# Performance work log

Measured on AMD Instinct MI355X. Metric: run time of the kernel, lower is better.

Reference implementation:

```python
import jax, jax.numpy as jnp
import numpy as np

H_K, H_V, DK, DV = 8, 16, 128, 128
HIDDEN = 2048
KDIM, VDIM = H_K * DK, H_V * DV          # 1024, 2048
CONV_DIM = 2 * KDIM + VDIM               # 4096
KS = 4                                   # conv kernel size
EPS = 1e-6


def setup_inputs() -> dict:
    key = jax.random.key(0)
    ks = jax.random.split(key, 8)
    B, S = 1, 1024
    return {
        "hidden_states": jax.random.normal(ks[0], (B, S, HIDDEN), jnp.float32),
        "W_qkvz": jax.random.uniform(ks[1], (HIDDEN, 2 * KDIM + 2 * VDIM), jnp.float32, -0.25, 0.25) * 0.1,
        "W_ba": jax.random.uniform(ks[2], (HIDDEN, 2 * H_V), jnp.float32, -0.25, 0.25),
        "conv_w": jax.random.normal(ks[3], (CONV_DIM, KS), jnp.float32) * 0.1,
        "dt_bias": jnp.ones((H_V,), jnp.float32),
        "A_log": jnp.log(jax.random.uniform(ks[4], (H_V,), jnp.float32, 1e-4, 16.0)),
        "norm_weight": jnp.ones((DV,), jnp.float32),
        "W_out": jax.random.uniform(ks[5], (VDIM, HIDDEN), jnp.float32, -0.06, 0.06),
    }


def _split_qkvz_ba(qkvz, ba):
    # mimic fix_query_key_value_ordering: per-k-head interleaved layout
    B, S, _ = qkvz.shape
    vpk = H_V // H_K
    qkvz = qkvz.reshape(B, S, H_K, 2 * DK + 2 * vpk * DV)
    q = qkvz[..., :DK]
    k = qkvz[..., DK:2 * DK]
    v = qkvz[..., 2 * DK:2 * DK + vpk * DV].reshape(B, S, H_V, DV)
    z = qkvz[..., 2 * DK + vpk * DV:].reshape(B, S, H_V, DV)
    ba = ba.reshape(B, S, H_K, 2 * vpk)
    b = ba[..., :vpk].reshape(B, S, H_V)
    a = ba[..., vpk:].reshape(B, S, H_V)
    return q, k, v, z, b, a


def _causal_conv_silu(x, w):
    # x: [B, S, C] ; w: [C, K] depthwise causal conv, then SiLU
    xt = jnp.swapaxes(x, 1, 2)                      # [B, C, S]
    xt = jnp.pad(xt, ((0, 0), (0, 0), (KS - 1, 0)))
    y = jax.lax.conv_general_dilated(
        xt, w[:, None, :], (1,), 'VALID',
        dimension_numbers=('NCH', 'OIH', 'NCH'),
        feature_group_count=w.shape[0])
    return jax.nn.silu(jnp.swapaxes(y, 1, 2))       # [B, S, C]


def _l2norm(x):
    return x * jax.lax.rsqrt(jnp.sum(x * x, axis=-1, keepdims=True) + 1e-6)


def _gated_delta_rule(q, k, v, g, beta):
    # q, k: [B,S,H,DK]; v: [B,S,H,DV]; g, beta: [B,S,H]
    B, S, H, _ = q.shape
    scale = DK ** -0.5
    q = _l2norm(q) * scale
    k = _l2norm(k)
    qs = jnp.moveaxis(q, 1, 0)   # [S,B,H,DK]
    ks = jnp.moveaxis(k, 1, 0)
    vs = jnp.moveaxis(v, 1, 0)
    gs = jnp.moveaxis(g, 1, 0)   # [S,B,H]
    bs = jnp.moveaxis(beta, 1, 0)
    S0 = jnp.zeros((B, H, DK, DV), q.dtype)

    def step(St, xs):
        qt, kt, vt, gt, bt = xs
        St = St * jnp.exp(gt)[..., None, None]
        pred = jnp.einsum('bhk,bhkv->bhv', kt, St)
        delta = (vt - pred) * bt[..., None]
        St = St + jnp.einsum('bhk,bhv->bhkv', kt, delta)
        o = jnp.einsum('bhk,bhkv->bhv', qt, St)
        return St, o

    _, o = jax.lax.scan(step, S0, (qs, ks, vs, gs, bs))
    return jnp.moveaxis(o, 0, 1)  # [B,S,H,DV]


def _gated_rmsnorm(x, z, w):
    # FLA FusedRMSNormGated (silu): rmsnorm(x)*w, gated by silu(z)
    var = jnp.mean(x * x, axis=-1, keepdims=True)
    return (x * jax.lax.rsqrt(var + EPS)) * w * jax.nn.silu(z)


def _forward(hidden_states, W_qkvz, W_ba, conv_w, dt_bias, A_log, norm_weight, W_out):
    B, S, _ = hidden_states.shape
    qkvz = hidden_states @ W_qkvz
    ba = hidden_states @ W_ba
    q, k, v, z, b, a = _split_qkvz_ba(qkvz, ba)
    mixed = jnp.concatenate([q.reshape(B, S, KDIM), k.reshape(B, S, KDIM),
                             v.reshape(B, S, VDIM)], axis=-1)
    mixed = _causal_conv_silu(mixed, conv_w)
    q = mixed[..., :KDIM].reshape(B, S, H_K, DK)
    k = mixed[..., KDIM:2 * KDIM].reshape(B, S, H_K, DK)
    v = mixed[..., 2 * KDIM:].reshape(B, S, H_V, DV)
    beta = jax.nn.sigmoid(b)
    g = -jnp.exp(A_log) * jax.nn.softplus(a + dt_bias)   # [B,S,H_V]
    rep = H_V // H_K
    q = jnp.repeat(q, rep, axis=2)
    k = jnp.repeat(k, rep, axis=2)
    o = _gated_delta_rule(q, k, v, g, beta)              # [B,S,H_V,DV]
    o = _gated_rmsnorm(o, z, norm_weight)
    return o.reshape(B, S, VDIM) @ W_out


def reference(hidden_states, W_qkvz, W_ba, conv_w, dt_bias, A_log, norm_weight, W_out):
    return _forward(hidden_states, W_qkvz, W_ba, conv_w, dt_bias, A_log, norm_weight, W_out)
```

## Files before the change

### kernel.cpp

```cpp
#include <hip/hip_runtime.h>
#include <hip/hip_bf16.h>
#include <math.h>


#define SEQ 1024
#define HID 2048
#define NQKVZ 6144

typedef __attribute__((ext_vector_type(8))) short short8;
typedef __attribute__((ext_vector_type(4))) float f32x4;

__device__ __forceinline__ unsigned short f2bf(float f) {
  __hip_bfloat16 h = __float2bfloat16(f);
  return *reinterpret_cast<unsigned short*>(&h);
}
__device__ __forceinline__ float bf2f(unsigned short u) {
  unsigned int x = ((unsigned int)u) << 16;
  return __int_as_float(x);
}

typedef __attribute__((address_space(3))) void lds_void;
typedef const __attribute__((address_space(1))) void g_void;
__device__ __forceinline__ void gload16(const void* g, void* l) {
  __builtin_amdgcn_global_load_lds((g_void*)g, (lds_void*)l, 16, 0, 0);
}

__global__ __launch_bounds__(256) void cast_bf16(const float* __restrict__ in,
                                                 unsigned short* __restrict__ out,
                                                 int n) {
  const int i = (blockIdx.x * 256 + threadIdx.x) * 4;
  if (i < n) {
    const float4 v = *(const float4*)&in[i];
    ushort4 o;
    o.x = f2bf(v.x); o.y = f2bf(v.y); o.z = f2bf(v.z); o.w = f2bf(v.w);
    *(ushort4*)&out[i] = o;
  }
}

__global__ __launch_bounds__(256) void transpose_cast2(const float* __restrict__ W1,
                                                       unsigned short* __restrict__ W1t,
                                                       const float* __restrict__ W2,
                                                       unsigned short* __restrict__ W2t) {
  __shared__ float tile[32][33];
  int bx = blockIdx.x;
  const float* W;
  unsigned short* Wt;
  int N;
  if (bx < 192) { W = W1; Wt = W1t; N = NQKVZ; }
  else          { W = W2; Wt = W2t; N = HID; bx -= 192; }
  const int n0 = bx * 32, k0 = blockIdx.y * 32;
  const int tx = threadIdx.x & 31, ty = threadIdx.x >> 5;
#pragma unroll
  for (int r = 0; r < 32; r += 8)
    tile[ty + r][tx] = W[(size_t)(k0 + ty + r) * N + n0 + tx];
  __syncthreads();
#pragma unroll
  for (int r = 0; r < 32; r += 8)
    Wt[(size_t)(n0 + ty + r) * HID + k0 + tx] = f2bf(tile[tx][ty + r]);
}

__global__ __launch_bounds__(256) void transpose_f32(const float* __restrict__ W,
                                                     float* __restrict__ Wt,
                                                     int K, int N) {
  __shared__ float tile[32][33];
  const int n0 = blockIdx.x * 32, k0 = blockIdx.y * 32;
  const int tx = threadIdx.x & 31, ty = threadIdx.x >> 5;
#pragma unroll
  for (int r = 0; r < 32; r += 8)
    tile[ty + r][tx] = W[(size_t)(k0 + ty + r) * N + n0 + tx];
  __syncthreads();
#pragma unroll
  for (int r = 0; r < 32; r += 8)
    Wt[(size_t)(n0 + ty + r) * K + k0 + tx] = tile[tx][ty + r];
}

#define SWZ(row) ((KF == 1) ? (((row) >> 1) & 3) : ((row) & 7))

template <int MF, int NF, int KF>
__global__ __launch_bounds__(256) void gemm_bf16(const unsigned short* __restrict__ A,
                                                 const unsigned short* __restrict__ Bt,
                                                 float* __restrict__ C,
                                                 int M, int N, int K) {
  constexpr int BM = 32 * MF, BN = 32 * NF, BK = 32 * KF;
  constexpr int RB  = BK * 2;
  constexpr int APW = (BM * KF / 16) / 4;
  constexpr int BPW = (BN * KF / 16) / 4;
  constexpr int RPG = 16 / KF;
  __shared__ unsigned short As[2][BM * BK];
  __shared__ unsigned short Bs[2][BN * BK];

  const int tid  = threadIdx.x;
  const int lane = tid & 63;
  const int w    = tid >> 6;
  const int wm   = w >> 1, wn = w & 1;
  const int row0 = blockIdx.y * BM, col0 = blockIdx.x * BN;

  const int lrow  = (KF == 1) ? (lane >> 2) : (lane >> 3);
  const int lslot = lane & (4 * KF - 1);
  const int arow  = lane & 15;

  f32x4 acc[MF][NF];
#pragma unroll
  for (int m = 0; m < MF; ++m)
#pragma unroll
    for (int n = 0; n < NF; ++n) acc[m][n] = (f32x4){0.f, 0.f, 0.f, 0.f};

  auto stage = [&](int bi, int kt) {
    const int ko = kt * BK;
#pragma unroll
    for (int u = 0; u < APW; ++u) {
      const int gu = w * APW + u;
      const int row = gu * RPG + lrow;
      const int sg = lslot ^ SWZ(row);
      gload16(A + (size_t)(row0 + row) * K + ko + sg * 8,
              (char*)As[bi] + gu * 1024 + lane * 16);
    }
#pragma unroll
    for (int u = 0; u < BPW; ++u) {
      const int gu = w * BPW + u;
      const int row = gu * RPG + lrow;
      const int sg = lslot ^ SWZ(row);
      gload16(Bt + (size_t)(col0 + row) * K + ko + sg * 8,
              (char*)Bs[bi] + gu * 1024 + lane * 16);
    }
  };

  stage(0, 0);
  __syncthreads();

  int cur = 0;
  const int nk = K / BK;
  for (int kt = 0; kt < nk; ++kt) {
    if (kt + 1 < nk) stage(cur ^ 1, kt + 1);

    const char* asb = (const char*)As[cur];
    const char* bsb = (const char*)Bs[cur];
    short8 af[MF][KF], bf[NF][KF];
#pragma unroll
    for (int m = 0; m < MF; ++m)
#pragma unroll
      for (int kk = 0; kk < KF; ++kk) {
        const int row = wm * (16 * MF) + m * 16 + arow;
        const int slot = kk * 4 + (lane >> 4);
        af[m][kk] = *(const short8*)(asb + row * RB + ((slot ^ SWZ(row)) * 16));
      }
#pragma unroll
    for (int n = 0; n < NF; ++n)
#pragma unroll
      for (int kk = 0; kk < KF; ++kk) {
        const int row = wn * (16 * NF) + n * 16 + arow;
        const int slot = kk * 4 + (lane >> 4);
        bf[n][kk] = *(const short8*)(bsb + row * RB + ((slot ^ SWZ(row)) * 16));
      }
#pragma unroll
    for (int m = 0; m < MF; ++m)
#pragma unroll
      for (int n = 0; n < NF; ++n)
#pragma unroll
        for (int kk = 0; kk < KF; ++kk)
          acc[m][n] = __builtin_amdgcn_mfma_f32_16x16x32_bf16(af[m][kk], bf[n][kk],
                                                              acc[m][n], 0, 0, 0);

    __syncthreads();
    cur ^= 1;
  }

#pragma unroll
  for (int m = 0; m < MF; ++m)
#pragma unroll
    for (int n = 0; n < NF; ++n) {
      const int r0 = row0 + wm * (16 * MF) + m * 16 + (lane >> 4) * 4;
      const int c  = col0 + wn * (16 * NF) + n * 16 + (lane & 15);
#pragma unroll
      for (int r = 0; r < 4; ++r)
        C[(size_t)(r0 + r) * N + c] = acc[m][n][r];
    }
}

__global__ __launch_bounds__(256) void ba_kernel(const float* __restrict__ X,
                                                 const float* __restrict__ Wbt,
                                                 const float* __restrict__ A_log,
                                                 const float* __restrict__ dt_bias,
                                                 float* __restrict__ gbuf,
                                                 float* __restrict__ bet) {
  const int col = threadIdx.x & 31;
  const int kg  = threadIdx.x >> 5;
  const int s0  = blockIdx.x * 4;
  const float* wp = Wbt + (size_t)col * HID + kg * 256;
  const float* xp = X + (size_t)s0 * HID + kg * 256;

  float a0 = 0.f, a1 = 0.f, a2 = 0.f, a3 = 0.f;
  for (int kk = 0; kk < 256; kk += 4) {
    const float4 w4 = *(const float4*)&wp[kk];
    const float4 x0 = *(const float4*)&xp[kk];
    const float4 x1 = *(const float4*)&xp[kk + HID];
    const float4 x2 = *(const float4*)&xp[kk + 2 * HID];
    const float4 x3 = *(const float4*)&xp[kk + 3 * HID];
    a0 += x0.x * w4.x + x0.y * w4.y + x0.z * w4.z + x0.w * w4.w;
    a1 += x1.x * w4.x + x1.y * w4.y + x1.z * w4.z + x1.w * w4.w;
    a2 += x2.x * w4.x + x2.y * w4.y + x2.z * w4.z + x2.w * w4.w;
    a3 += x3.x * w4.x + x3.y * w4.y + x3.z * w4.z + x3.w * w4.w;
  }
  __shared__ float red[4][32][9];
  red[0][col][kg] = a0;
  red[1][col][kg] = a1;
  red[2][col][kg] = a2;
  red[3][col][kg] = a3;
  __syncthreads();
  if (threadIdx.x < 128) {
    const int r = threadIdx.x >> 5;
    const int c = threadIdx.x & 31;
    float acc = 0.f;
#pragma unroll
    for (int g = 0; g < 8; ++g) acc += red[r][c][g];
    const int s = s0 + r;
    const int hk = c >> 2, j = c & 3;
    if (j < 2) {
      bet[s * 16 + hk * 2 + j] = 1.f / (1.f + expf(-acc));
    } else {
      const int vh = hk * 2 + (j - 2);
      const float x = acc + dt_bias[vh];
      const float sp = (x > 20.f) ? x : log1pf(expf(x));
      gbuf[s * 16 + vh] = -expf(A_log[vh]) * sp;
    }
  }
}

#define NT 512
__global__ __launch_bounds__(NT) void chunk_prep(
    const float* __restrict__ qkvz, const float* __restrict__ conv_w,
    const float* __restrict__ gbuf, const float* __restrict__ bet,
    unsigned short* __restrict__ Tg, unsigned short* __restrict__ Gg,
    unsigned short* __restrict__ Wtg, unsigned short* __restrict__ Qtg,
    unsigned short* __restrict__ Khg, float* __restrict__ bvg,
    float* __restrict__ esg) {
  const int h  = blockIdx.x >> 4;
  const int c  = blockIdx.x & 15;
  const int hk = h >> 1;
  const int tid = threadIdx.x;
  const int lane = tid & 63;
  const int w    = tid >> 6;
  const int lr   = lane & 15;
  const int lk   = lane >> 4;

  __shared__ float raw[67][128];
  __shared__ unsigned short Kb[64 * 128];
  __shared__ unsigned short Qb[64 * 128];
  __shared__ unsigned short Bm[64][64];
  __shared__ float cg[64];
  __shared__ float btl[64];

  const int s0 = c * 64;
  const int qcol0 = hk * 768;
  const int kcol0 = hk * 768 + 128;
  const int vcol0 = hk * 768 + 256 + (h & 1) * 128;

  if (tid < 64) {
    float g = gbuf[(s0 + tid) * 16 + h];
#pragma unroll
    for (int d = 1; d < 64; d <<= 1) {
      const float o = __shfl_up(g, d);
      if (tid >= d) g += o;
    }
    cg[tid] = g;
    btl[tid] = bet[(s0 + tid) * 16 + h];
  }

  float4 rq[5], rk[5], rv[5];

#define ISSUE(col0_, rg)                                                      \
  _Pragma("unroll")                                                           \
  for (int ii = 0; ii < 5; ++ii) {                                            \
    const int idx = tid + NT * ii;                                            \
    if (idx < 67 * 32) {                                                      \
      const int r = idx >> 5, cq = (idx & 31) * 4;                            \
      const int sr = s0 - 3 + r;                                              \
      if (sr >= 0)                                                            \
        rg[ii] = *(const float4*)&qkvz[(size_t)sr * NQKVZ + (col0_) + cq];    \
      else { rg[ii].x = 0.f; rg[ii].y = 0.f; rg[ii].z = 0.f; rg[ii].w = 0.f; }\
    }                                                                         \
  }

#define WRITE(rg)                                                             \
  _Pragma("unroll")                                                           \
  for (int ii = 0; ii < 5; ++ii) {                                            \
    const int idx = tid + NT * ii;                                            \
    if (idx < 67 * 32) {                                                      \
      const int r = idx >> 5, cq = (idx & 31) * 4;                            \
      *(float4*)&raw[r][cq] = rg[ii];                                         \
    }                                                                         \
  }

#define CONV_TO(dst, wbase, isq)                                              \
  for (int n = 0; n < 4; ++n) {                                               \
    const int idx = tid + NT * n;                                             \
    const int row = idx >> 5;                                                 \
    const int col = (idx & 31) * 4;                                           \
    float wgt[4][4];                                                          \
    _Pragma("unroll")                                                         \
    for (int x = 0; x < 4; ++x) {                                             \
      const float4 a = *(const float4*)&conv_w[((wbase) + hk * 128 + col + x) * 4]; \
      wgt[x][0] = a.x; wgt[x][1] = a.y; wgt[x][2] = a.z; wgt[x][3] = a.w;     \
    }                                                                         \
    float4 ac = {0.f, 0.f, 0.f, 0.f};                                         \
    _Pragma("unroll")                                                         \
    for (int j = 0; j < 4; ++j) {                                             \
      const float4 xr = *(const float4*)&raw[row + j][col];                   \
      ac.x = fmaf(wgt[0][j], xr.x, ac.x); ac.y = fmaf(wgt[1][j], xr.y, ac.y); \
      ac.z = fmaf(wgt[2][j], xr.z, ac.z); ac.w = fmaf(wgt[3][j], xr.w, ac.w); \
    }                                                                         \
    float4 y;                                                                 \
    y.x = ac.x / (1.f + __expf(-ac.x)); y.y = ac.y / (1.f + __expf(-ac.y));   \
    y.z = ac.z / (1.f + __expf(-ac.z)); y.w = ac.w / (1.f + __expf(-ac.w));   \
    float ss = y.x * y.x + y.y * y.y + y.z * y.z + y.w * y.w;                 \
    _Pragma("unroll")                                                         \
    for (int m = 1; m <= 16; m <<= 1) ss += __shfl_xor(ss, m);                \
    float sc = rsqrtf(ss + 1e-6f);                                            \
    if (isq) sc *= 0.08838834764831845f;                                      \
    const int boff = row * 256 + ((col * 2) ^ ((row & 7) << 4));              \
    ushort4 o = {f2bf(y.x * sc), f2bf(y.y * sc), f2bf(y.z * sc), f2bf(y.w * sc)}; \
    *(ushort4*)((char*)(dst) + boff) = o;                                     \
  }

  ISSUE(qcol0, rq);
  WRITE(rq);
  __syncthreads();
  ISSUE(kcol0, rk);
  CONV_TO(Qb, 0, true);
  __syncthreads();
  WRITE(rk);
  __syncthreads();
  ISSUE(vcol0, rv);
  CONV_TO(Kb, 1024, false);
  __syncthreads();
  WRITE(rv);

  const bool isK = (w < 4);
  const int w4 = w & 3;
  f32x4 dacc[4];
#pragma unroll
  for (int ct = 0; ct < 4; ++ct) dacc[ct] = (f32x4){0.f, 0.f, 0.f, 0.f};
  {
    const int rowA = 16 * w4 + lr;
    const int swA  = (rowA & 7) << 4;
    const char* Ab = isK ? (const char*)Kb : (const char*)Qb;
#pragma unroll
    for (int ks = 0; ks < 4; ++ks) {
      const int kb = ks * 64 + lk * 16;
      const short8 a = *(const short8*)(Ab + rowA * 256 + (kb ^ swA));
#pragma unroll
      for (int ct = 0; ct < 4; ++ct) {
        const int rowB = ct * 16 + lr;
        const short8 bK = *(const short8*)((char*)Kb + rowB * 256 + (kb ^ ((rowB & 7) << 4)));
        dacc[ct] = __builtin_amdgcn_mfma_f32_16x16x32_bf16(a, bK, dacc[ct], 0, 0, 0);
      }
    }
  }
#pragma unroll
  for (int ct = 0; ct < 4; ++ct) {
#pragma unroll
    for (int r = 0; r < 4; ++r) {
      const int i = 16 * w4 + lk * 4 + r;
      const int j = ct * 16 + lr;
      const float e = __expf(cg[i] - cg[j]);
      if (isK) Bm[i][j] = f2bf((j < i) ? btl[i] * e * dacc[ct][r] : 0.f);
      else     Gg[(size_t)blockIdx.x * 4096 + i * 64 + j] =
                   f2bf((j <= i) ? e * dacc[ct][r] : 0.f);
    }
  }
  __syncthreads();

  const float cglast = cg[63];
  if (w == 0) {
    const int l = lane;
    float Tc[64];
#pragma unroll
    for (int i = 0; i < 64; ++i) {
      float v = (i == l) ? 1.f : 0.f;
#pragma unroll
      for (int j = 0; j < i; ++j) v -= bf2f(Bm[i][j]) * Tc[j];
      Tc[i] = v;
    }
#pragma unroll
    for (int i = 0; i < 64; ++i)
      Tg[(size_t)blockIdx.x * 4096 + i * 64 + l] = f2bf(Tc[i]);
    if (lane == 0) esg[blockIdx.x] = __expf(cglast);
  } else {
    const int t2 = tid - 64;
    for (int idx = t2; idx < 2048; idx += 448) {
      const int i = idx >> 5;
      const int dk = (idx & 31) * 4;
      const int boff = i * 256 + ((dk * 2) ^ ((i & 7) << 4));
      const ushort4 kq = *(const ushort4*)((char*)Kb + boff);
      const ushort4 qq = *(const ushort4*)((char*)Qb + boff);
      const float ei = __expf(cg[i]);
      const float wi = btl[i] * ei;
      ushort4 wo = {f2bf(wi * bf2f(kq.x)), f2bf(wi * bf2f(kq.y)),
                    f2bf(wi * bf2f(kq.z)), f2bf(wi * bf2f(kq.w))};
      ushort4 qo = {f2bf(ei * bf2f(qq.x)), f2bf(ei * bf2f(qq.y)),
                    f2bf(ei * bf2f(qq.z)), f2bf(ei * bf2f(qq.w))};
      *(ushort4*)&Wtg[(size_t)blockIdx.x * 8192 + i * 128 + dk] = wo;
      *(ushort4*)&Qtg[(size_t)blockIdx.x * 8192 + i * 128 + dk] = qo;

      float wv[4][4];
#pragma unroll
      for (int x = 0; x < 4; ++x) {
        const float4 a = *(const float4*)&conv_w[(2048 + h * 128 + dk + x) * 4];
        wv[x][0] = a.x; wv[x][1] = a.y; wv[x][2] = a.z; wv[x][3] = a.w;
      }
      float4 va = {0.f, 0.f, 0.f, 0.f};
#pragma unroll
      for (int j = 0; j < 4; ++j) {
        const float4 xv = *(const float4*)&raw[i + j][dk];
        va.x = fmaf(wv[0][j], xv.x, va.x); va.y = fmaf(wv[1][j], xv.y, va.y);
        va.z = fmaf(wv[2][j], xv.z, va.z); va.w = fmaf(wv[3][j], xv.w, va.w);
      }
      float4 bv4;
      bv4.x = btl[i] * va.x / (1.f + __expf(-va.x));
      bv4.y = btl[i] * va.y / (1.f + __expf(-va.y));
      bv4.z = btl[i] * va.z / (1.f + __expf(-va.z));
      bv4.w = btl[i] * va.w / (1.f + __expf(-va.w));
      *(float4*)&bvg[(size_t)blockIdx.x * 8192 + i * 128 + dk] = bv4;
    }
    for (int lin = t2; lin < 8192; lin += 448) {
      const int dk = lin >> 6, i = lin & 63;
      const unsigned short kraw =
          *(const unsigned short*)((char*)Kb + i * 256 + ((dk * 2) ^ ((i & 7) << 4)));
      Khg[(size_t)blockIdx.x * 8192 + lin] = f2bf(__expf(cglast - cg[i]) * bf2f(kraw));
    }
  }
#undef ISSUE
#undef WRITE
#undef CONV_TO
}
#undef NT

struct SFrags {
  short8 wf[4];
  short8 tf[2];
  short8 qf[4];
  short8 gf[2];
  short8 kh[2][2];
  float  bv[4];
  float  es;
};

__device__ __forceinline__ void sload(SFrags& F,
    const unsigned short* __restrict__ Tg, const unsigned short* __restrict__ Gg,
    const unsigned short* __restrict__ Wtg, const unsigned short* __restrict__ Qtg,
    const unsigned short* __restrict__ Khg, const float* __restrict__ bvg,
    const float* __restrict__ esg,
    size_t base, int w, int lr, int lk, int dv0) {
  const unsigned short* T_  = Tg  + base * 4096;
  const unsigned short* G_  = Gg  + base * 4096;
  const unsigned short* W_  = Wtg + base * 8192;
  const unsigned short* Q_  = Qtg + base * 8192;
  const unsigned short* Kh_ = Khg + base * 8192;
  const float* bv_ = bvg + base * 8192;
#pragma unroll
  for (int ks = 0; ks < 4; ++ks) {
    F.wf[ks] = *(const short8*)(W_ + (16 * w + lr) * 128 + ks * 32 + lk * 8);
    F.qf[ks] = *(const short8*)(Q_ + (16 * w + lr) * 128 + ks * 32 + lk * 8);
  }
#pragma unroll
  for (int ks = 0; ks < 2; ++ks) {
    F.tf[ks]    = *(const short8*)(T_ + (16 * w + lr) * 64 + ks * 32 + lk * 8);
    F.gf[ks]    = *(const short8*)(G_ + (16 * w + lr) * 64 + ks * 32 + lk * 8);
    F.kh[0][ks] = *(const short8*)(Kh_ + (32 * w + lr) * 64 + ks * 32 + lk * 8);
    F.kh[1][ks] = *(const short8*)(Kh_ + (32 * w + 16 + lr) * 64 + ks * 32 + lk * 8);
  }
#pragma unroll
  for (int r = 0; r < 4; ++r)
    F.bv[r] = bv_[(16 * w + lk * 4 + r) * 128 + dv0 + lr];
  F.es = esg[base];
}

__global__ __launch_bounds__(256) void scan_rec(
    const unsigned short* __restrict__ Tg, const unsigned short* __restrict__ Gg,
    const unsigned short* __restrict__ Wtg, const unsigned short* __restrict__ Qtg,
    const unsigned short* __restrict__ Khg, const float* __restrict__ bvg,
    const float* __restrict__ esg, float* __restrict__ obuf) {
  const int h   = blockIdx.x & 15;
  const int dvb = blockIdx.x >> 4;
  const int dv0 = dvb * 16;
  const int tid = threadIdx.x;
  const int lane = tid & 63;
  const int w   = tid >> 6;
  const int lr  = lane & 15;
  const int lk  = lane >> 4;

  __shared__ unsigned short Sb[16][136];
  __shared__ unsigned short Ub[16][72];
  __shared__ unsigned short Db[16][72];

  for (int n = tid; n < 16 * 136 / 2; n += 256) ((unsigned int*)Sb)[n] = 0u;

  f32x4 sacc0 = {0.f, 0.f, 0.f, 0.f};
  f32x4 sacc1 = {0.f, 0.f, 0.f, 0.f};

  SFrags fA, fB;
  sload(fA, Tg, Gg, Wtg, Qtg, Khg, bvg, esg, (size_t)h * 16, w, lr, lk, dv0);
  __syncthreads();

#define SCAN_CHUNK(F, c)                                                      \
  {                                                                           \
    short8 sb[4];                                                             \
    _Pragma("unroll")                                                         \
    for (int ks = 0; ks < 4; ++ks)                                            \
      sb[ks] = *(const short8*)(&Sb[lr][ks * 32 + lk * 8]);                   \
    f32x4 au = {0.f, 0.f, 0.f, 0.f};                                          \
    _Pragma("unroll")                                                         \
    for (int ks = 0; ks < 4; ++ks)                                            \
      au = __builtin_amdgcn_mfma_f32_16x16x32_bf16(F.wf[ks], sb[ks], au, 0, 0, 0); \
    {                                                                         \
      ushort4 pk;                                                             \
      _Pragma("unroll")                                                       \
      for (int r = 0; r < 4; ++r)                                             \
        ((unsigned short*)&pk)[r] = f2bf(F.bv[r] - au[r]);                    \
      *(ushort4*)&Ub[lr][16 * w + lk * 4] = pk;                               \
    }                                                                         \
    __syncthreads();                                                          \
    f32x4 ad = {0.f, 0.f, 0.f, 0.f};                                          \
    _Pragma("unroll")                                                         \
    for (int ks = 0; ks < 2; ++ks) {                                          \
      const short8 ub = *(const short8*)(&Ub[lr][ks * 32 + lk * 8]);          \
      ad = __builtin_amdgcn_mfma_f32_16x16x32_bf16(F.tf[ks], ub, ad, 0, 0, 0); \
    }                                                                         \
    {                                                                         \
      ushort4 pk;                                                             \
      _Pragma("unroll")                                                       \
      for (int r = 0; r < 4; ++r) ((unsigned short*)&pk)[r] = f2bf(ad[r]);    \
      *(ushort4*)&Db[lr][16 * w + lk * 4] = pk;                               \
    }                                                                         \
    __syncthreads();                                                          \
    short8 dbf[2];                                                            \
    _Pragma("unroll")                                                         \
    for (int ks = 0; ks < 2; ++ks)                                            \
      dbf[ks] = *(const short8*)(&Db[lr][ks * 32 + lk * 8]);                  \
    f32x4 ao = {0.f, 0.f, 0.f, 0.f};                                          \
    _Pragma("unroll")                                                         \
    for (int ks = 0; ks < 4; ++ks)                                            \
      ao = __builtin_amdgcn_mfma_f32_16x16x32_bf16(F.qf[ks], sb[ks], ao, 0, 0, 0); \
    _Pragma("unroll")                                                         \
    for (int ks = 0; ks < 2; ++ks)                                            \
      ao = __builtin_amdgcn_mfma_f32_16x16x32_bf16(F.gf[ks], dbf[ks], ao, 0, 0, 0); \
    _Pragma("unroll")                                                         \
    for (int r = 0; r < 4; ++r) {                                             \
      const int i = 16 * w + lk * 4 + r;                                      \
      obuf[((size_t)((c) * 64 + i) * 16 + h) * 128 + dv0 + lr] = ao[r];       \
    }                                                                         \
    sacc0 *= F.es;                                                            \
    sacc1 *= F.es;                                                            \
    _Pragma("unroll")                                                         \
    for (int ks = 0; ks < 2; ++ks) {                                          \
      sacc0 = __builtin_amdgcn_mfma_f32_16x16x32_bf16(F.kh[0][ks], dbf[ks], sacc0, 0, 0, 0); \
      sacc1 = __builtin_amdgcn_mfma_f32_16x16x32_bf16(F.kh[1][ks], dbf[ks], sacc1, 0, 0, 0); \
    }                                                                         \
    {                                                                         \
      ushort4 p0, p1;                                                         \
      _Pragma("unroll")                                                       \
      for (int r = 0; r < 4; ++r) {                                           \
        ((unsigned short*)&p0)[r] = f2bf(sacc0[r]);                           \
        ((unsigned short*)&p1)[r] = f2bf(sacc1[r]);                           \
      }                                                                       \
      *(ushort4*)&Sb[lr][32 * w + lk * 4] = p0;                               \
      *(ushort4*)&Sb[lr][32 * w + 16 + lk * 4] = p1;                          \
    }                                                                         \
    __syncthreads();                                                          \
  }

  for (int c = 0; c < 16; c += 2) {
    const int c1 = (c + 1 < 15) ? c + 1 : 15;
    const int c2 = (c + 2 < 15) ? c + 2 : 15;
    sload(fB, Tg, Gg, Wtg, Qtg, Khg, bvg, esg, (size_t)h * 16 + c1, w, lr, lk, dv0);
    SCAN_CHUNK(fA, c);
    sload(fA, Tg, Gg, Wtg, Qtg, Khg, bvg, esg, (size_t)h * 16 + c2, w, lr, lk, dv0);
    SCAN_CHUNK(fB, c + 1);
  }
#undef SCAN_CHUNK
}

__global__ __launch_bounds__(128) void rmsnorm_kernel(const float* __restrict__ obuf,
                                                      const float* __restrict__ qkvz,
                                                      const float* __restrict__ nw,
                                                      unsigned short* __restrict__ on) {
  const int vh = blockIdx.x;
  const int s  = blockIdx.y;
  const int d  = threadIdx.x;

  const float x = obuf[((size_t)s * 16 + vh) * 128 + d];
  float ss = x * x;
#pragma unroll
  for (int m = 1; m < 64; m <<= 1) ss += __shfl_xor(ss, m);
  __shared__ float red[2];
  if ((threadIdx.x & 63) == 0) red[threadIdx.x >> 6] = ss;
  __syncthreads();
  const float tot = red[0] + red[1];

  const float z = qkvz[(size_t)s * NQKVZ + (vh >> 1) * 768 + 512 + (vh & 1) * 128 + d];
  const float y = x * rsqrtf(tot * (1.f / 128.f) + 1e-6f) * nw[d] *
                  (z / (1.f + expf(-z)));
  on[(size_t)s * 2048 + vh * 128 + d] = f2bf(y);
}

extern "C" void kernel_launch(void* const* d_in, const int* in_sizes, int n_in,
                              void* d_out, int out_size, void* d_ws, size_t ws_size,
                              hipStream_t stream) {
  const float* hid     = (const float*)d_in[0];
  const float* W_qkvz  = (const float*)d_in[1];
  const float* W_ba    = (const float*)d_in[2];
  const float* conv_w  = (const float*)d_in[3];
  const float* dt_bias = (const float*)d_in[4];
  const float* A_log   = (const float*)d_in[5];
  const float* norm_w  = (const float*)d_in[6];
  const float* W_out   = (const float*)d_in[7];
  float* out = (float*)d_out;

  char* ws = (char*)d_ws;
  float* qkvz = (float*)ws;                 ws += (size_t)SEQ * NQKVZ * 4;
  char* region2 = ws;                       ws += (size_t)HID * NQKVZ * 2;
  unsigned short* W1t = (unsigned short*)region2;
  float* obuf = (float*)(region2 + 16777216);
  unsigned short* Xb = (unsigned short*)ws; ws += (size_t)SEQ * HID * 2;
  unsigned short* on_bf = Xb;
  unsigned short* W2t = (unsigned short*)ws; ws += (size_t)HID * HID * 2;
  float* gbuf = (float*)ws;                  ws += (size_t)SEQ * 16 * 4;
  float* bet  = (float*)ws;                  ws += (size_t)SEQ * 16 * 4;
  unsigned short* Tg  = (unsigned short*)ws; ws += (size_t)256 * 4096 * 2;
  unsigned short* Gg  = (unsigned short*)ws; ws += (size_t)256 * 4096 * 2;
  unsigned short* Wtg = (unsigned short*)ws; ws += (size_t)256 * 8192 * 2;
  unsigned short* Qtg = (unsigned short*)ws; ws += (size_t)256 * 8192 * 2;
  unsigned short* Khg = (unsigned short*)ws; ws += (size_t)256 * 8192 * 2;
  float* bvg          = (float*)ws;          ws += (size_t)256 * 8192 * 4;
  float* esg          = (float*)ws;          ws += 256 * 4;
  float* Wbt          = (float*)ws;          ws += (size_t)32 * HID * 4;

  cast_bf16<<<dim3(SEQ * HID / 1024), 256, 0, stream>>>(hid, Xb, SEQ * HID);
  transpose_cast2<<<dim3(256, 64), 256, 0, stream>>>(W_qkvz, W1t, W_out, W2t);
  transpose_f32<<<dim3(1, HID / 32), 256, 0, stream>>>(W_ba, Wbt, HID, 32);
  ba_kernel<<<dim3(SEQ / 4), 256, 0, stream>>>(hid, Wbt, A_log, dt_bias, gbuf, bet);
  gemm_bf16<2, 4, 2><<<dim3(NQKVZ / 128, SEQ / 64), 256, 0, stream>>>(Xb, W1t, qkvz,
                                                                      SEQ, NQKVZ, HID);
  chunk_prep<<<dim3(256), 512, 0, stream>>>(qkvz, conv_w, gbuf, bet,
                                            Tg, Gg, Wtg, Qtg, Khg, bvg, esg);
  scan_rec<<<dim3(128), 256, 0, stream>>>(Tg, Gg, Wtg, Qtg, Khg, bvg, esg, obuf);
  rmsnorm_kernel<<<dim3(16, SEQ), 128, 0, stream>>>(obuf, qkvz, norm_w, on_bf);
  gemm_bf16<2, 2, 1><<<dim3(HID / 64, SEQ / 64), 256, 0, stream>>>(on_bf, W2t, out,
                                                                   SEQ, HID, HID);
}
```

Before: 176.8 us.

## Merge prep kernels into one launch, restructure rmsnorm, deepen out-proj K tile

Four preprocessing launches (input cast, two weight transposes, the W_ba transpose and the ba projection) are folded into one kernel that branches on block index. The ba projection now reads W_ba directly with strided loads instead of going through a transposed copy. The rmsnorm kernel handles a whole sequence row per 256-thread block, looping over heads instead of launching one block per head. The output GEMM moves from KF=1 to KF=2. These target launch overhead and tail effects, at the cost of more per-block loop syncs and uncoalesced W_ba reads.

Measured after the change: 184.3 us. +4.2%, slower.

```diff
diff --git a/kernel.cpp b/kernel.cpp
--- a/kernel.cpp
+++ b/kernel.cpp
@@ -25,53 +25,96 @@
   __builtin_amdgcn_global_load_lds((g_void*)g, (lds_void*)l, 16, 0, 0);
 }
 
-__global__ __launch_bounds__(256) void cast_bf16(const float* __restrict__ in,
-                                                 unsigned short* __restrict__ out,
-                                                 int n) {
-  const int i = (blockIdx.x * 256 + threadIdx.x) * 4;
-  if (i < n) {
-    const float4 v = *(const float4*)&in[i];
+__global__ __launch_bounds__(256) void prep_kernel(
+    const float* __restrict__ hid, const float* __restrict__ W_qkvz,
+    const float* __restrict__ W_out, const float* __restrict__ W_ba,
+    const float* __restrict__ A_log, const float* __restrict__ dt_bias,
+    unsigned short* __restrict__ Xb, unsigned short* __restrict__ W1t,
+    unsigned short* __restrict__ W2t,
+    float* __restrict__ gbuf, float* __restrict__ bet) {
+  __shared__ float tile[32][33];
+  __shared__ float red[4][32][9];
+  int bx = blockIdx.x;
+  const int tx = threadIdx.x & 31, ty = threadIdx.x >> 5;
+
+  if (bx < 12288) {
+    const int n0 = (bx % 192) * 32, k0 = (bx / 192) * 32;
+#pragma unroll
+    for (int r = 0; r < 32; r += 8)
+      tile[ty + r][tx] = W_qkvz[(size_t)(k0 + ty + r) * NQKVZ + n0 + tx];
+    __syncthreads();
+#pragma unroll
+    for (int r = 0; r < 32; r += 8)
+      W1t[(size_t)(n0 + ty + r) * HID + k0 + tx] = f2bf(tile[tx][ty + r]);
+    return;
+  }
+  bx -= 12288;
+  if (bx < 4096) {
+    const int n0 = (bx & 63) * 32, k0 = (bx >> 6) * 32;
+#pragma unroll
+    for (int r = 0; r < 32; r += 8)
+      tile[ty + r][tx] = W_out[(size_t)(k0 + ty + r) * HID + n0 + tx];
+    __syncthreads();
+#pragma unroll
+    for (int r = 0; r < 32; r += 8)
+      W2t[(size_t)(n0 + ty + r) * HID + k0 + tx] = f2bf(tile[tx][ty + r]);
+    return;
+  }
+  bx -= 4096;
+  if (bx < 2048) {
+    const int i = (bx * 256 + threadIdx.x) * 4;
+    const float4 v = *(const float4*)&hid[i];
     ushort4 o;
     o.x = f2bf(v.x); o.y = f2bf(v.y); o.z = f2bf(v.z); o.w = f2bf(v.w);
-    *(ushort4*)&out[i] = o;
-  }
-}
-
-__global__ __launch_bounds__(256) void transpose_cast2(const float* __restrict__ W1,
-                                                       unsigned short* __restrict__ W1t,
-                                                       const float* __restrict__ W2,
-                                                       unsigned short* __restrict__ W2t) {
-  __shared__ float tile[32][33];
-  int bx = blockIdx.x;
-  const float* W;
-  unsigned short* Wt;
-  int N;
-  if (bx < 192) { W = W1; Wt = W1t; N = NQKVZ; }
-  else          { W = W2; Wt = W2t; N = HID; bx -= 192; }
-  const int n0 = bx * 32, k0 = blockIdx.y * 32;
-  const int tx = threadIdx.x & 31, ty = threadIdx.x >> 5;
-#pragma unroll
-  for (int r = 0; r < 32; r += 8)
-    tile[ty + r][tx] = W[(size_t)(k0 + ty + r) * N + n0 + tx];
-  __syncthreads();
-#pragma unroll
-  for (int r = 0; r < 32; r += 8)
-    Wt[(size_t)(n0 + ty + r) * HID + k0 + tx] = f2bf(tile[tx][ty + r]);
-}
-
-__global__ __launch_bounds__(256) void transpose_f32(const float* __restrict__ W,
-                                                     float* __restrict__ Wt,
-                                                     int K, int N) {
-  __shared__ float tile[32][33];
-  const int n0 = blockIdx.x * 32, k0 = blockIdx.y * 32;
-  const int tx = threadIdx.x & 31, ty = threadIdx.x >> 5;
-#pragma unroll
-  for (int r = 0; r < 32; r += 8)
-    tile[ty + r][tx] = W[(size_t)(k0 + ty + r) * N + n0 + tx];
-  __syncthreads();
-#pragma unroll
-  for (int r = 0; r < 32; r += 8)
-    Wt[(size_t)(n0 + ty + r) * K + k0 + tx] = tile[tx][ty + r];
+    *(ushort4*)&Xb[i] = o;
+    return;
+  }
+  bx -= 2048;
+  {
+    const int col = threadIdx.x & 31;
+    const int kg  = threadIdx.x >> 5;
+    const int s0  = bx * 4;
+    const float* wp = W_ba + (size_t)(kg * 256) * 32 + col;
+    const float* xp = hid + (size_t)s0 * HID + kg * 256;
+
+    float a0 = 0.f, a1 = 0.f, a2 = 0.f, a3 = 0.f;
+    for (int kk = 0; kk < 256; kk += 4) {
+      const float w0 = wp[(kk + 0) * 32];
+      const float w1 = wp[(kk + 1) * 32];
+      const float w2 = wp[(kk + 2) * 32];
+      const float w3 = wp[(kk + 3) * 32];
+      const float4 x0 = *(const float4*)&xp[kk];
+      const float4 x1 = *(const float4*)&xp[kk + HID];
+      const float4 x2 = *(const float4*)&xp[kk + 2 * HID];
+      const float4 x3 = *(const float4*)&xp[kk + 3 * HID];
+      a0 += x0.x * w0 + x0.y * w1 + x0.z * w2 + x0.w * w3;
+      a1 += x1.x * w0 + x1.y * w1 + x1.z * w2 + x1.w * w3;
+      a2 += x2.x * w0 + x2.y * w1 + x2.z * w2 + x2.w * w3;
+      a3 += x3.x * w0 + x3.y * w1 + x3.z * w2 + x3.w * w3;
+    }
+    red[0][col][kg] = a0;
+    red[1][col][kg] = a1;
+    red[2][col][kg] = a2;
+    red[3][col][kg] = a3;
+    __syncthreads();
+    if (threadIdx.x < 128) {
+      const int r = threadIdx.x >> 5;
+      const int c = threadIdx.x & 31;
+      float acc = 0.f;
+#pragma unroll
+      for (int g = 0; g < 8; ++g) acc += red[r][c][g];
+      const int s = s0 + r;
+      const int hk = c >> 2, j = c & 3;
+      if (j < 2) {
+        bet[s * 16 + hk * 2 + j] = 1.f / (1.f + expf(-acc));
+      } else {
+        const int vh = hk * 2 + (j - 2);
+        const float x = acc + dt_bias[vh];
+        const float sp = (x > 20.f) ? x : log1pf(expf(x));
+        gbuf[s * 16 + vh] = -expf(A_log[vh]) * sp;
+      }
+    }
+  }
 }
 
 #define SWZ(row) ((KF == 1) ? (((row) >> 1) & 3) : ((row) & 7))
@@ -175,55 +218,6 @@
       for (int r = 0; r < 4; ++r)
         C[(size_t)(r0 + r) * N + c] = acc[m][n][r];
     }
-}
-
-__global__ __launch_bounds__(256) void ba_kernel(const float* __restrict__ X,
-                                                 const float* __restrict__ Wbt,
-                                                 const float* __restrict__ A_log,
-                                                 const float* __restrict__ dt_bias,
-                                                 float* __restrict__ gbuf,
-                                                 float* __restrict__ bet) {
-  const int col = threadIdx.x & 31;
-  const int kg  = threadIdx.x >> 5;
-  const int s0  = blockIdx.x * 4;
-  const float* wp = Wbt + (size_t)col * HID + kg * 256;
-  const float* xp = X + (size_t)s0 * HID + kg * 256;
-
-  float a0 = 0.f, a1 = 0.f, a2 = 0.f, a3 = 0.f;
-  for (int kk = 0; kk < 256; kk += 4) {
-    const float4 w4 = *(const float4*)&wp[kk];
-    const float4 x0 = *(const float4*)&xp[kk];
-    const float4 x1 = *(const float4*)&xp[kk + HID];
-    const float4 x2 = *(const float4*)&xp[kk + 2 * HID];
-    const float4 x3 = *(const float4*)&xp[kk + 3 * HID];
-    a0 += x0.x * w4.x + x0.y * w4.y + x0.z * w4.z + x0.w * w4.w;
-    a1 += x1.x * w4.x + x1.y * w4.y + x1.z * w4.z + x1.w * w4.w;
-    a2 += x2.x * w4.x + x2.y * w4.y + x2.z * w4.z + x2.w * w4.w;
-    a3 += x3.x * w4.x + x3.y * w4.y + x3.z * w4.z + x3.w * w4.w;
-  }
-  __shared__ float red[4][32][9];
-  red[0][col][kg] = a0;
-  red[1][col][kg] = a1;
-  red[2][col][kg] = a2;
-  red[3][col][kg] = a3;
-  __syncthreads();
-  if (threadIdx.x < 128) {
-    const int r = threadIdx.x >> 5;
-    const int c = threadIdx.x & 31;
-    float acc = 0.f;
-#pragma unroll
-    for (int g = 0; g < 8; ++g) acc += red[r][c][g];
-    const int s = s0 + r;
-    const int hk = c >> 2, j = c & 3;
-    if (j < 2) {
-      bet[s * 16 + hk * 2 + j] = 1.f / (1.f + expf(-acc));
-    } else {
-      const int vh = hk * 2 + (j - 2);
-      const float x = acc + dt_bias[vh];
-      const float sp = (x > 20.f) ? x : log1pf(expf(x));
-      gbuf[s * 16 + vh] = -expf(A_log[vh]) * sp;
-    }
-  }
 }
 
 #define NT 512
@@ -580,27 +574,31 @@
 #undef SCAN_CHUNK
 }
 
-__global__ __launch_bounds__(128) void rmsnorm_kernel(const float* __restrict__ obuf,
+__global__ __launch_bounds__(256) void rmsnorm_kernel(const float* __restrict__ obuf,
                                                       const float* __restrict__ qkvz,
                                                       const float* __restrict__ nw,
                                                       unsigned short* __restrict__ on) {
-  const int vh = blockIdx.x;
-  const int s  = blockIdx.y;
-  const int d  = threadIdx.x;
-
-  const float x = obuf[((size_t)s * 16 + vh) * 128 + d];
-  float ss = x * x;
-#pragma unroll
-  for (int m = 1; m < 64; m <<= 1) ss += __shfl_xor(ss, m);
-  __shared__ float red[2];
-  if ((threadIdx.x & 63) == 0) red[threadIdx.x >> 6] = ss;
-  __syncthreads();
-  const float tot = red[0] + red[1];
-
-  const float z = qkvz[(size_t)s * NQKVZ + (vh >> 1) * 768 + 512 + (vh & 1) * 128 + d];
-  const float y = x * rsqrtf(tot * (1.f / 128.f) + 1e-6f) * nw[d] *
-                  (z / (1.f + expf(-z)));
-  on[(size_t)s * 2048 + vh * 128 + d] = f2bf(y);
+  const int s    = blockIdx.x;
+  const int half = threadIdx.x >> 7;
+  const int d    = threadIdx.x & 127;
+  __shared__ float red[4];
+
+  for (int it = 0; it < 8; ++it) {
+    const int vh = it * 2 + half;
+    const float x = obuf[((size_t)s * 16 + vh) * 128 + d];
+    float ss = x * x;
+#pragma unroll
+    for (int m = 1; m < 64; m <<= 1) ss += __shfl_xor(ss, m);
+    if ((threadIdx.x & 63) == 0) red[threadIdx.x >> 6] = ss;
+    __syncthreads();
+    const float tot = red[half * 2] + red[half * 2 + 1];
+
+    const float z = qkvz[(size_t)s * NQKVZ + (vh >> 1) * 768 + 512 + (vh & 1) * 128 + d];
+    const float y = x * rsqrtf(tot * (1.f / 128.f) + 1e-6f) * nw[d] *
+                    (z / (1.f + expf(-z)));
+    on[(size_t)s * 2048 + vh * 128 + d] = f2bf(y);
+    __syncthreads();
+  }
 }
 
 extern "C" void kernel_launch(void* const* d_in, const int* in_sizes, int n_in,
@@ -633,18 +631,16 @@
   unsigned short* Khg = (unsigned short*)ws; ws += (size_t)256 * 8192 * 2;
   float* bvg          = (float*)ws;          ws += (size_t)256 * 8192 * 4;
   float* esg          = (float*)ws;          ws += 256 * 4;
-  float* Wbt          = (float*)ws;          ws += (size_t)32 * HID * 4;
-
-  cast_bf16<<<dim3(SEQ * HID / 1024), 256, 0, stream>>>(hid, Xb, SEQ * HID);
-  transpose_cast2<<<dim3(256, 64), 256, 0, stream>>>(W_qkvz, W1t, W_out, W2t);
-  transpose_f32<<<dim3(1, HID / 32), 256, 0, stream>>>(W_ba, Wbt, HID, 32);
-  ba_kernel<<<dim3(SEQ / 4), 256, 0, stream>>>(hid, Wbt, A_log, dt_bias, gbuf, bet);
+
+  prep_kernel<<<dim3(18688), 256, 0, stream>>>(hid, W_qkvz, W_out, W_ba,
+                                               A_log, dt_bias,
+                                               Xb, W1t, W2t, gbuf, bet);
   gemm_bf16<2, 4, 2><<<dim3(NQKVZ / 128, SEQ / 64), 256, 0, stream>>>(Xb, W1t, qkvz,
                                                                       SEQ, NQKVZ, HID);
   chunk_prep<<<dim3(256), 512, 0, stream>>>(qkvz, conv_w, gbuf, bet,
                                             Tg, Gg, Wtg, Qtg, Khg, bvg, esg);
   scan_rec<<<dim3(128), 256, 0, stream>>>(Tg, Gg, Wtg, Qtg, Khg, bvg, esg, obuf);
-  rmsnorm_kernel<<<dim3(16, SEQ), 128, 0, stream>>>(obuf, qkvz, norm_w, on_bf);
-  gemm_bf16<2, 2, 1><<<dim3(HID / 64, SEQ / 64), 256, 0, stream>>>(on_bf, W2t, out,
+  rmsnorm_kernel<<<dim3(SEQ), 256, 0, stream>>>(obuf, qkvz, norm_w, on_bf);
+  gemm_bf16<2, 2, 2><<<dim3(HID / 64, SEQ / 64), 256, 0, stream>>>(on_bf, W2t, out,
                                                                    SEQ, HID, HID);
 }
```

## Widen weight transpose tiles, batch rmsnorm per row, bump out-GEMM K tile

Applied to the files above, without the earlier changes.

The bf16 weight transpose now uses 64x64 tiles with float4 loads and ushort4 stores instead of scalar 32x32 accesses, which cuts block count and widens memory transactions. The W_ba transpose is specialised to its fixed 32-column shape. The rmsnorm kernel processes all 16 heads of a sequence row in one 256-thread block, launching far fewer, larger blocks at the cost of extra barriers per iteration. The output GEMM switches to a K-fold of 2 to halve the number of k-loop iterations and barriers. The 64x65 LDS tile read by column with a 4-wide stride may cause bank conflicts.

New measurement: 173.5 us. Within noise of the previous version (-1.8%).

```diff
diff --git a/kernel.cpp b/kernel.cpp
--- a/kernel.cpp
+++ b/kernel.cpp
@@ -41,37 +41,96 @@
                                                        unsigned short* __restrict__ W1t,
                                                        const float* __restrict__ W2,
                                                        unsigned short* __restrict__ W2t) {
-  __shared__ float tile[32][33];
+  __shared__ float tile[64][65];
   int bx = blockIdx.x;
   const float* W;
   unsigned short* Wt;
   int N;
-  if (bx < 192) { W = W1; Wt = W1t; N = NQKVZ; }
-  else          { W = W2; Wt = W2t; N = HID; bx -= 192; }
-  const int n0 = bx * 32, k0 = blockIdx.y * 32;
+  if (bx < 96) { W = W1; Wt = W1t; N = NQKVZ; }
+  else         { W = W2; Wt = W2t; N = HID; bx -= 96; }
+  const int n0 = bx * 64, k0 = blockIdx.y * 64;
+  const int tc = (threadIdx.x & 15) * 4;
+  const int tr = threadIdx.x >> 4;
+
+#pragma unroll
+  for (int rr = 0; rr < 64; rr += 16) {
+    const float4 v = *(const float4*)&W[(size_t)(k0 + tr + rr) * N + n0 + tc];
+    *(float4*)&tile[tr + rr][tc] = v;
+  }
+  __syncthreads();
+#pragma unroll
+  for (int rr = 0; rr < 64; rr += 16) {
+    const int r = tr + rr;
+    ushort4 o;
+    o.x = f2bf(tile[tc + 0][r]);
+    o.y = f2bf(tile[tc + 1][r]);
+    o.z = f2bf(tile[tc + 2][r]);
+    o.w = f2bf(tile[tc + 3][r]);
+    *(ushort4*)&Wt[(size_t)(n0 + r) * HID + k0 + tc] = o;
+  }
+}
+
+__global__ __launch_bounds__(256) void transpose_f32(const float* __restrict__ W,
+                                                     float* __restrict__ Wt) {
+  __shared__ float tile[32][33];
+  const int k0 = blockIdx.x * 32;
   const int tx = threadIdx.x & 31, ty = threadIdx.x >> 5;
 #pragma unroll
   for (int r = 0; r < 32; r += 8)
-    tile[ty + r][tx] = W[(size_t)(k0 + ty + r) * N + n0 + tx];
+    tile[ty + r][tx] = W[(size_t)(k0 + ty + r) * 32 + tx];
   __syncthreads();
 #pragma unroll
   for (int r = 0; r < 32; r += 8)
-    Wt[(size_t)(n0 + ty + r) * HID + k0 + tx] = f2bf(tile[tx][ty + r]);
-}
-
-__global__ __launch_bounds__(256) void transpose_f32(const float* __restrict__ W,
-                                                     float* __restrict__ Wt,
-                                                     int K, int N) {
-  __shared__ float tile[32][33];
-  const int n0 = blockIdx.x * 32, k0 = blockIdx.y * 32;
-  const int tx = threadIdx.x & 31, ty = threadIdx.x >> 5;
-#pragma unroll
-  for (int r = 0; r < 32; r += 8)
-    tile[ty + r][tx] = W[(size_t)(k0 + ty + r) * N + n0 + tx];
-  __syncthreads();
-#pragma unroll
-  for (int r = 0; r < 32; r += 8)
-    Wt[(size_t)(n0 + ty + r) * K + k0 + tx] = tile[tx][ty + r];
+    Wt[(size_t)(ty + r) * HID + k0 + tx] = tile[tx][ty + r];
+}
+
+__global__ __launch_bounds__(256) void ba_kernel(const float* __restrict__ X,
+                                                 const float* __restrict__ Wbt,
+                                                 const float* __restrict__ A_log,
+                                                 const float* __restrict__ dt_bias,
+                                                 float* __restrict__ gbuf,
+                                                 float* __restrict__ bet) {
+  const int col = threadIdx.x & 31;
+  const int kg  = threadIdx.x >> 5;
+  const int s0  = blockIdx.x * 4;
+  const float* wp = Wbt + (size_t)col * HID + kg * 256;
+  const float* xp = X + (size_t)s0 * HID + kg * 256;
+
+  float a0 = 0.f, a1 = 0.f, a2 = 0.f, a3 = 0.f;
+  for (int kk = 0; kk < 256; kk += 4) {
+    const float4 w4 = *(const float4*)&wp[kk];
+    const float4 x0 = *(const float4*)&xp[kk];
+    const float4 x1 = *(const float4*)&xp[kk + HID];
+    const float4 x2 = *(const float4*)&xp[kk + 2 * HID];
+    const float4 x3 = *(const float4*)&xp[kk + 3 * HID];
+    a0 += x0.x * w4.x + x0.y * w4.y + x0.z * w4.z + x0.w * w4.w;
+    a1 += x1.x * w4.x + x1.y * w4.y + x1.z * w4.z + x1.w * w4.w;
+    a2 += x2.x * w4.x + x2.y * w4.y + x2.z * w4.z + x2.w * w4.w;
+    a3 += x3.x * w4.x + x3.y * w4.y + x3.z * w4.z + x3.w * w4.w;
+  }
+  __shared__ float red[4][32][9];
+  red[0][col][kg] = a0;
+  red[1][col][kg] = a1;
+  red[2][col][kg] = a2;
+  red[3][col][kg] = a3;
+  __syncthreads();
+  if (threadIdx.x < 128) {
+    const int r = threadIdx.x >> 5;
+    const int c = threadIdx.x & 31;
+    float acc = 0.f;
+#pragma unroll
+    for (int g = 0; g < 8; ++g) acc += red[r][c][g];
+    const int s = s0 + r;
+    const int hk = c >> 2, j = c & 3;
+    if (j < 2) {
+      bet[s * 16 + hk * 2 + j] = 1.f / (1.f + expf(-acc));
+    } else {
+      const int vh = hk * 2 + (j - 2);
+      const float x = acc + dt_bias[vh];
+      const float sp = (x > 20.f) ? x : log1pf(expf(x));
+      gbuf[s * 16 + vh] = -expf(A_log[vh]) * sp;
+    }
+  }
 }
 
 #define SWZ(row) ((KF == 1) ? (((row) >> 1) & 3) : ((row) & 7))
@@ -175,55 +234,6 @@
       for (int r = 0; r < 4; ++r)
         C[(size_t)(r0 + r) * N + c] = acc[m][n][r];
     }
-}
-
-__global__ __launch_bounds__(256) void ba_kernel(const float* __restrict__ X,
-                                                 const float* __restrict__ Wbt,
-                                                 const float* __restrict__ A_log,
-                                                 const float* __restrict__ dt_bias,
-                                                 float* __restrict__ gbuf,
-                                                 float* __restrict__ bet) {
-  const int col = threadIdx.x & 31;
-  const int kg  = threadIdx.x >> 5;
-  const int s0  = blockIdx.x * 4;
-  const float* wp = Wbt + (size_t)col * HID + kg * 256;
-  const float* xp = X + (size_t)s0 * HID + kg * 256;
-
-  float a0 = 0.f, a1 = 0.f, a2 = 0.f, a3 = 0.f;
-  for (int kk = 0; kk < 256; kk += 4) {
-    const float4 w4 = *(const float4*)&wp[kk];
-    const float4 x0 = *(const float4*)&xp[kk];
-    const float4 x1 = *(const float4*)&xp[kk + HID];
-    const float4 x2 = *(const float4*)&xp[kk + 2 * HID];
-    const float4 x3 = *(const float4*)&xp[kk + 3 * HID];
-    a0 += x0.x * w4.x + x0.y * w4.y + x0.z * w4.z + x0.w * w4.w;
-    a1 += x1.x * w4.x + x1.y * w4.y + x1.z * w4.z + x1.w * w4.w;
-    a2 += x2.x * w4.x + x2.y * w4.y + x2.z * w4.z + x2.w * w4.w;
-    a3 += x3.x * w4.x + x3.y * w4.y + x3.z * w4.z + x3.w * w4.w;
-  }
-  __shared__ float red[4][32][9];
-  red[0][col][kg] = a0;
-  red[1][col][kg] = a1;
-  red[2][col][kg] = a2;
-  red[3][col][kg] = a3;
-  __syncthreads();
-  if (threadIdx.x < 128) {
-    const int r = threadIdx.x >> 5;
-    const int c = threadIdx.x & 31;
-    float acc = 0.f;
-#pragma unroll
-    for (int g = 0; g < 8; ++g) acc += red[r][c][g];
-    const int s = s0 + r;
-    const int hk = c >> 2, j = c & 3;
-    if (j < 2) {
-      bet[s * 16 + hk * 2 + j] = 1.f / (1.f + expf(-acc));
-    } else {
-      const int vh = hk * 2 + (j - 2);
-      const float x = acc + dt_bias[vh];
-      const float sp = (x > 20.f) ? x : log1pf(expf(x));
-      gbuf[s * 16 + vh] = -expf(A_log[vh]) * sp;
-    }
-  }
 }
 
 #define NT 512
@@ -580,27 +590,31 @@
 #undef SCAN_CHUNK
 }
 
-__global__ __launch_bounds__(128) void rmsnorm_kernel(const float* __restrict__ obuf,
+__global__ __launch_bounds__(256) void rmsnorm_kernel(const float* __restrict__ obuf,
                                                       const float* __restrict__ qkvz,
                                                       const float* __restrict__ nw,
                                                       unsigned short* __restrict__ on) {
-  const int vh = blockIdx.x;
-  const int s  = blockIdx.y;
-  const int d  = threadIdx.x;
-
-  const float x = obuf[((size_t)s * 16 + vh) * 128 + d];
-  float ss = x * x;
-#pragma unroll
-  for (int m = 1; m < 64; m <<= 1) ss += __shfl_xor(ss, m);
-  __shared__ float red[2];
-  if ((threadIdx.x & 63) == 0) red[threadIdx.x >> 6] = ss;
-  __syncthreads();
-  const float tot = red[0] + red[1];
-
-  const float z = qkvz[(size_t)s * NQKVZ + (vh >> 1) * 768 + 512 + (vh & 1) * 128 + d];
-  const float y = x * rsqrtf(tot * (1.f / 128.f) + 1e-6f) * nw[d] *
-                  (z / (1.f + expf(-z)));
-  on[(size_t)s * 2048 + vh * 128 + d] = f2bf(y);
+  const int s    = blockIdx.x;
+  const int half = threadIdx.x >> 7;
+  const int d    = threadIdx.x & 127;
+  __shared__ float red[4];
+
+  for (int it = 0; it < 8; ++it) {
+    const int vh = it * 2 + half;
+    const float x = obuf[((size_t)s * 16 + vh) * 128 + d];
+    float ss = x * x;
+#pragma unroll
+    for (int m = 1; m < 64; m <<= 1) ss += __shfl_xor(ss, m);
+    if ((threadIdx.x & 63) == 0) red[threadIdx.x >> 6] = ss;
+    __syncthreads();
+    const float tot = red[half * 2] + red[half * 2 + 1];
+
+    const float z = qkvz[(size_t)s * NQKVZ + (vh >> 1) * 768 + 512 + (vh & 1) * 128 + d];
+    const float y = x * rsqrtf(tot * (1.f / 128.f) + 1e-6f) * nw[d] *
+                    (z / (1.f + expf(-z)));
+    on[(size_t)s * 2048 + vh * 128 + d] = f2bf(y);
+    __syncthreads();
+  }
 }
 
 extern "C" void kernel_launch(void* const* d_in, const int* in_sizes, int n_in,
@@ -636,15 +650,15 @@
   float* Wbt          = (float*)ws;          ws += (size_t)32 * HID * 4;
 
   cast_bf16<<<dim3(SEQ * HID / 1024), 256, 0, stream>>>(hid, Xb, SEQ * HID);
-  transpose_cast2<<<dim3(256, 64), 256, 0, stream>>>(W_qkvz, W1t, W_out, W2t);
-  transpose_f32<<<dim3(1, HID / 32), 256, 0, stream>>>(W_ba, Wbt, HID, 32);
+  transpose_cast2<<<dim3(128, 32), 256, 0, stream>>>(W_qkvz, W1t, W_out, W2t);
+  transpose_f32<<<dim3(HID / 32), 256, 0, stream>>>(W_ba, Wbt);
   ba_kernel<<<dim3(SEQ / 4), 256, 0, stream>>>(hid, Wbt, A_log, dt_bias, gbuf, bet);
   gemm_bf16<2, 4, 2><<<dim3(NQKVZ / 128, SEQ / 64), 256, 0, stream>>>(Xb, W1t, qkvz,
                                                                       SEQ, NQKVZ, HID);
   chunk_prep<<<dim3(256), 512, 0, stream>>>(qkvz, conv_w, gbuf, bet,
                                             Tg, Gg, Wtg, Qtg, Khg, bvg, esg);
   scan_rec<<<dim3(128), 256, 0, stream>>>(Tg, Gg, Wtg, Qtg, Khg, bvg, esg, obuf);
-  rmsnorm_kernel<<<dim3(16, SEQ), 128, 0, stream>>>(obuf, qkvz, norm_w, on_bf);
-  gemm_bf16<2, 2, 1><<<dim3(HID / 64, SEQ / 64), 256, 0, stream>>>(on_bf, W2t, out,
+  rmsnorm_kernel<<<dim3(SEQ), 256, 0, stream>>>(obuf, qkvz, norm_w, on_bf);
+  gemm_bf16<2, 2, 2><<<dim3(HID / 64, SEQ / 64), 256, 0, stream>>>(on_bf, W2t, out,
                                                                    SEQ, HID, HID);
 }
```
